# Performance work log

Hardware: AMD Instinct MI355X
Metric: run time of the kernel (lower is better)

The kernel has to match this reference:

```python
import jax, jax.numpy as jnp
import numpy as np

B, H, W, C = 32, 56, 56, 512
HEADS, WS, SS = 16, 7, 3
N = WS * WS            # window area = 49
HD = C // HEADS        # head dim = 32
HID = 4 * C            # mlp hidden = 2048
nWh, nWw = H // WS, W // WS
nW = nWh * nWw


def _rel_pos_index():
    # static (N, N) int index into relative_position_bias_table
    coords = np.stack(np.meshgrid(np.arange(WS), np.arange(WS), indexing='ij'))  # (2, WS, WS)
    cf = coords.reshape(2, -1)                       # (2, N)
    rel = (cf[:, :, None] - cf[:, None, :]).transpose(1, 2, 0).copy()  # (N, N, 2)
    rel[:, :, 0] += WS - 1
    rel[:, :, 1] += WS - 1
    rel[:, :, 0] *= 2 * WS - 1
    return rel.sum(-1)  # (N, N)


def _attn_mask():
    # static shifted-window attention mask, (nW, N, N) with 0 / -100
    img = np.zeros((H, W))
    cnt = 0
    for h0, h1 in ((0, H - WS), (H - WS, H - SS), (H - SS, H)):
        for w0, w1 in ((0, W - WS), (W - WS, W - SS), (W - SS, W)):
            img[h0:h1, w0:w1] = cnt
            cnt += 1
    mw = img.reshape(nWh, WS, nWw, WS).transpose(0, 2, 1, 3).reshape(-1, N)  # (nW, N)
    diff = mw[:, None, :] - mw[:, :, None]
    return np.where(diff != 0, -100.0, 0.0).astype(np.float32)

_REL_IDX = _rel_pos_index()
_MASK = _attn_mask()


def _ln(x, g, b, eps=1e-5):
    mu = x.mean(-1, keepdims=True)
    var = ((x - mu) ** 2).mean(-1, keepdims=True)
    return (x - mu) * jax.lax.rsqrt(var + eps) * g + b


def setup_inputs() -> dict:
    key = jax.random.key(0)
    ks = jax.random.split(key, 8)
    s = lambda k, shape: jax.random.normal(k, shape, jnp.float32) * 0.02
    return {
        'x': jax.random.normal(ks[0], (B, H, W, C), jnp.float32),
        'norm1_g': jnp.ones((C,), jnp.float32), 'norm1_b': jnp.zeros((C,), jnp.float32),
        'qkv_w': s(ks[1], (3 * C, C)), 'qkv_b': jnp.zeros((3 * C,), jnp.float32),
        'rel_pos_table': s(ks[2], ((2 * WS - 1) ** 2, HEADS)),
        'proj_w': s(ks[3], (C, C)), 'proj_b': jnp.zeros((C,), jnp.float32),
        'norm2_g': jnp.ones((C,), jnp.float32), 'norm2_b': jnp.zeros((C,), jnp.float32),
        'fc1_w': s(ks[4], (HID, C)), 'fc1_b': jnp.zeros((HID,), jnp.float32),
        'fc2_w': s(ks[5], (C, HID)), 'fc2_b': jnp.zeros((C,), jnp.float32),
    }


def reference(x, norm1_g, norm1_b, qkv_w, qkv_b, rel_pos_table, proj_w, proj_b,
              norm2_g, norm2_b, fc1_w, fc1_b, fc2_w, fc2_b):
    shortcut = x
    y = _ln(x, norm1_g, norm1_b)
    # cyclic shift
    y = jnp.roll(y, (-SS, -SS), axis=(1, 2))
    # window partition -> (B*nW, N, C)
    yw = y.reshape(B, nWh, WS, nWw, WS, C).transpose(0, 1, 3, 2, 4, 5).reshape(B * nW, N, C)
    # qkv projection
    qkv = yw @ qkv_w.T + qkv_b
    qkv = qkv.reshape(B * nW, N, 3, HEADS, HD).transpose(2, 0, 3, 1, 4)
    q, k, v = qkv[0], qkv[1], qkv[2]              # each (B*nW, HEADS, N, HD)
    scale = HD ** -0.5
    attn = jnp.einsum('bhqd,bhkd->bhqk', q * scale, k)  # (B*nW, HEADS, N, N)
    # relative position bias gather
    bias = rel_pos_table[jnp.asarray(_REL_IDX.reshape(-1))].reshape(N, N, HEADS)
    attn = attn + bias.transpose(2, 0, 1)[None]
    # shifted-window mask
    attn = attn.reshape(B, nW, HEADS, N, N) + jnp.asarray(_MASK)[None, :, None]
    attn = jax.nn.softmax(attn.reshape(B * nW, HEADS, N, N), axis=-1)
    o = jnp.einsum('bhqk,bhkd->bhqd', attn, v)
    o = o.transpose(0, 2, 1, 3).reshape(B * nW, N, C)
    o = o @ proj_w.T + proj_b
    # window reverse + reverse shift
    o = o.reshape(B, nWh, nWw, WS, WS, C).transpose(0, 1, 3, 2, 4, 5).reshape(B, H, W, C)
    o = jnp.roll(o, (SS, SS), axis=(1, 2))
    x = shortcut + o
    # MLP
    h = _ln(x, norm2_g, norm2_b)
    h = jax.nn.gelu(h @ fc1_w.T + fc1_b, approximate=False)
    h = h @ fc2_w.T + fc2_b
    return x + h
```

## Files before the change

### kernel.cpp

```cpp
#include <hip/hip_runtime.h>

#define Bb   32
#define Hh   56
#define Ww_  56
#define Cc   512
#define HEADS 16
#define WS   7
#define SS   3
#define Nn   49
#define HD   32
#define HID  2048
#define NWIN 2048
#define NTOK 100352
#define NTOKP 100416

typedef __attribute__((ext_vector_type(4))) float f32x4;
typedef __attribute__((ext_vector_type(8))) short bf16x8;

#define AS1 __attribute__((address_space(1)))
#define AS3 __attribute__((address_space(3)))

__device__ __forceinline__ ushort f2bf(float x) {
  union { float f; unsigned u; } un; un.f = x;
  unsigned u = un.u;
  return (ushort)((u + 0x7fffu + ((u >> 16) & 1u)) >> 16);
}

__device__ __forceinline__ void cvt_frag_seg(const float* __restrict__ s, ushort* __restrict__ d,
                                             int N, int K, int tid0, int stride) {
  int nch = (N * K) >> 3;
  int kc = K >> 3;
  int kkt = K >> 5;
  for (int c = tid0; c < nch; c += stride) {
    int row = c / kc, col8 = c - row * kc;
    int n0 = row >> 4, l15 = row & 15;
    int kk = col8 >> 2, lhi = col8 & 3;
    int lane = (lhi << 4) | l15;
    const float* sp = s + (size_t)c * 8;
    ushort* dp = d + (((size_t)(n0 * kkt + kk) * 64 + lane) * 8);
    #pragma unroll
    for (int e = 0; e < 8; ++e) dp[e] = f2bf(sp[e]);
  }
}

__global__ void cvtwf_kern(const float* __restrict__ s0, ushort* __restrict__ d0,
                           const float* __restrict__ s1, ushort* __restrict__ d1,
                           const float* __restrict__ s2, ushort* __restrict__ d2,
                           const float* __restrict__ s3, ushort* __restrict__ d3) {
  int tid0 = blockIdx.x * 256 + threadIdx.x;
  int stride = gridDim.x * 256;
  cvt_frag_seg(s0, d0, 1536, 512, tid0, stride);
  cvt_frag_seg(s1, d1, 512, 512, tid0, stride);
  cvt_frag_seg(s2, d2, 2048, 512, tid0, stride);
  cvt_frag_seg(s3, d3, 512, 2048, tid0, stride);
}

__global__ void prep_bias_kern(const float* __restrict__ table, float* __restrict__ be2) {
  int idx = blockIdx.x * 256 + threadIdx.x;
  int h = idx >> 12, q = (idx >> 6) & 63, t = idx & 63;
  int l15 = t >> 2, n = t & 3;
  int key = n * 16 + l15;
  float v = 0.f;
  if (q < Nn && key < Nn) {
    int qi = q / 7, qj = q - qi * 7;
    int ki = key / 7, kj = key - ki * 7;
    v = table[((qi - ki + 6) * 13 + (qj - kj + 6)) * HEADS + h];
  }
  be2[idx] = v;
}

template<int MODE>
__global__ __launch_bounds__(256) void ln_kern(const float* __restrict__ x,
    const float* __restrict__ g, const float* __restrict__ bsh,
    ushort* __restrict__ out)
{
  int row  = blockIdx.x * 4 + (threadIdx.x >> 6);
  int lane = threadIdx.x & 63;
  const float* src;
  if (MODE == 0) {
    unsigned w = (unsigned)row / 49u, n = (unsigned)row - w * 49u;
    unsigned bb = w >> 6, wi = w & 63;
    unsigned wh = wi >> 3, ww = wi & 7;
    unsigned i = n / 7u, j = n - i * 7u;
    unsigned sr = wh * 7 + i + SS; if (sr >= Hh) sr -= Hh;
    unsigned sc = ww * 7 + j + SS; if (sc >= Ww_) sc -= Ww_;
    src = x + ((size_t)(bb * Hh + sr) * Ww_ + sc) * Cc;
  } else {
    src = x + (size_t)row * Cc;
  }
  int c = lane * 8;
  f32x4 v0 = *(const f32x4*)(src + c);
  f32x4 v1 = *(const f32x4*)(src + c + 4);
  float s = 0.f, s2 = 0.f;
  #pragma unroll
  for (int e = 0; e < 4; ++e) { s += v0[e]; s2 += v0[e]*v0[e]; s += v1[e]; s2 += v1[e]*v1[e]; }
  #pragma unroll
  for (int off = 32; off; off >>= 1) { s += __shfl_xor(s, off); s2 += __shfl_xor(s2, off); }
  float mu = s * (1.f / 512.f);
  float rstd = rsqrtf(s2 * (1.f / 512.f) - mu * mu + 1e-5f);
  bf16x8 r;
  #pragma unroll
  for (int e = 0; e < 8; ++e) {
    float xv = (e < 4) ? v0[e] : v1[e - 4];
    r[e] = (short)f2bf((xv - mu) * rstd * g[c + e] + bsh[c + e]);
  }
  *(bf16x8*)(out + (size_t)row * Cc + c) = r;
}

template<int EPI>
__global__ __launch_bounds__(256, 2) void gemm_kern(
    const ushort* __restrict__ A, const ushort* __restrict__ Bf,
    const float* __restrict__ bias, int M, int N, int K,
    void* __restrict__ outp, const float* __restrict__ resid,
    ushort* __restrict__ qb, ushort* __restrict__ kb, ushort* __restrict__ vb)
{
  __shared__ ushort As[2][128 * 64];
  const int tid = threadIdx.x;
  const int wave = tid >> 6, lane = tid & 63;
  const int l15 = lane & 15, lhi = lane >> 4;
  const int sw7 = l15 & 7;

  int gx = gridDim.x;
  int nwg = gx * gridDim.y;
  int orig = blockIdx.y * gx + blockIdx.x;
  int cpx = nwg >> 3;
  int wg = (orig & 7) * cpx + (orig >> 3);
  int bx = wg % gx, by = wg / gx;
  const int brow = by * 128, bcol = bx * 128;

  const int wr = (wave >> 1) * 64, wc = (wave & 1) * 64;

  const int srow = lane >> 3;
  const int schk = ((lane & 7) ^ srow) * 8;
  const ushort* aG = A + (size_t)(brow + srow) * K + schk;

  const int kkt = K >> 5;
  const int nb0 = (bcol + wc) >> 4;
  const ushort* bW = Bf + (size_t)nb0 * kkt * 512 + (size_t)lane * 8;

  auto stageA = [&](int kt, int sl) {
    #pragma unroll
    for (int s = 0; s < 4; ++s) {
      int rg = (s * 4 + wave) * 8;
      __builtin_amdgcn_global_load_lds(
        (const AS1 void*)(aG + (size_t)rg * K + kt * 64),
        (AS3 void*)&As[sl][rg * 64], 16, 0, 0);
    }
  };

  f32x4 acc[4][4];
  #pragma unroll
  for (int m = 0; m < 4; ++m)
    #pragma unroll
    for (int n = 0; n < 4; ++n)
      acc[m][n] = (f32x4){0.f, 0.f, 0.f, 0.f};

  const int nt = K >> 6;

  stageA(0, 0);
  __syncthreads();

  for (int t = 0; t < nt; ++t) {
    const int sl = t & 1;
    bf16x8 bfr[2][4];
    #pragma unroll
    for (int kk = 0; kk < 2; ++kk)
      #pragma unroll
      for (int n = 0; n < 4; ++n)
        bfr[kk][n] = *(const bf16x8*)(bW + ((size_t)n * kkt + t * 2 + kk) * 512);
    if (t + 1 < nt) stageA(t + 1, sl ^ 1);
    const ushort* Ap = As[sl];
    #pragma unroll
    for (int kk = 0; kk < 2; ++kk) {
      bf16x8 af[4];
      #pragma unroll
      for (int m = 0; m < 4; ++m)
        af[m] = *(const bf16x8*)&Ap[(wr + m * 16 + l15) * 64 + (((kk * 4 + lhi) ^ sw7)) * 8];
      #pragma unroll
      for (int m = 0; m < 4; ++m)
        #pragma unroll
        for (int n = 0; n < 4; ++n)
          acc[m][n] = __builtin_amdgcn_mfma_f32_16x16x32_bf16(af[m], bfr[kk][n], acc[m][n], 0, 0, 0);
    }
    __syncthreads();
  }

  float bv[4];
  #pragma unroll
  for (int n = 0; n < 4; ++n) bv[n] = bias[bcol + wc + n * 16 + l15];
  #pragma unroll
  for (int m = 0; m < 4; ++m) {
    int rbase = brow + wr + m * 16 + lhi * 4;
    #pragma unroll
    for (int n = 0; n < 4; ++n) {
      int cc = bcol + wc + n * 16 + l15;
      #pragma unroll
      for (int j = 0; j < 4; ++j) {
        unsigned r = (unsigned)(rbase + j);
        float v = acc[m][n][j] + bv[n];
        if (EPI == 0) {
          int part = cc >> 9, head = (cc >> 5) & 15, d = cc & 31;
          ushort bvs = f2bf(v);
          if (part == 0)      qb[((size_t)head * NTOKP + r) * 32 + d] = bvs;
          else if (part == 1) kb[((size_t)head * NTOKP + r) * 32 + d] = bvs;
          else {
            unsigned w = r / 49u, nn = r - w * 49u;
            vb[(((size_t)(w * HEADS + head)) * 32 + d) * 64 + nn] = bvs;
          }
        } else if (EPI == 1) {
          float u2 = v * (1.5957691216f + 0.0713548162f * v * v);
          float gl = __fdividef(v, 1.0f + __expf(-u2));
          ((ushort*)outp)[(size_t)r * N + cc] = f2bf(gl);
        } else if (EPI == 2) {
          unsigned w = r / 49u, nn = r - w * 49u;
          unsigned bb = w >> 6, wi = w & 63;
          unsigned wh = wi >> 3, ww = wi & 7;
          unsigned ii = nn / 7u, jj = nn - ii * 7u;
          unsigned dr = wh * 7 + ii + SS; if (dr >= Hh) dr -= Hh;
          unsigned dc = ww * 7 + jj + SS; if (dc >= Ww_) dc -= Ww_;
          size_t p = ((size_t)bb * Hh + dr) * Ww_ + dc;
          ((float*)outp)[p * Cc + cc] = resid[p * Cc + cc] + v;
        } else {
          float* o = (float*)outp;
          size_t idx = (size_t)r * Cc + cc;
          o[idx] = o[idx] + v;
        }
      }
    }
  }
}

__global__ __launch_bounds__(256) void attn_kern(
    const ushort* __restrict__ qb, const ushort* __restrict__ kb,
    const ushort* __restrict__ vb, const float* __restrict__ be2,
    ushort* __restrict__ o_win)
{
  __shared__ ushort P[4][4096];
  const int wv = threadIdx.x >> 6, lane = threadIdx.x & 63;
  const int l15 = lane & 15, lhi = lane >> 4;
  const int w = blockIdx.x;
  const int head = blockIdx.y * 4 + wv;
  const int wi = w & 63, whh = wi >> 3, www = wi & 7;
  ushort* Pl = P[wv];

  int krg[4];
  #pragma unroll
  for (int n = 0; n < 4; ++n) {
    int key = n * 16 + l15;
    int rg = -1;
    if (key < Nn) {
      int ki = key / 7, kj = key - ki * 7;
      int rr = whh * 7 + ki, cc = www * 7 + kj;
      rg = (rr < 49 ? 0 : (rr < 53 ? 1 : 2)) * 3 + (cc < 49 ? 0 : (cc < 53 ? 1 : 2));
    }
    krg[n] = rg;
  }
  int qrg[4][4];
  #pragma unroll
  for (int m = 0; m < 4; ++m)
    #pragma unroll
    for (int j = 0; j < 4; ++j) {
      int q = m * 16 + lhi * 4 + j;
      int rg = -2;
      if (q < Nn) {
        int qi = q / 7, qj = q - qi * 7;
        int rr = whh * 7 + qi, cc = www * 7 + qj;
        rg = (rr < 49 ? 0 : (rr < 53 ? 1 : 2)) * 3 + (cc < 49 ? 0 : (cc < 53 ? 1 : 2));
      }
      qrg[m][j] = rg;
    }

  const ushort* qp = qb + ((size_t)head * NTOKP + (size_t)w * 49) * 32;
  const ushort* kp = kb + ((size_t)head * NTOKP + (size_t)w * 49) * 32;
  const ushort* vp = vb + (size_t)(w * HEADS + head) * 2048;
  const float*  bep = be2 + head * 4096;

  bf16x8 qf[4], kf[4];
  #pragma unroll
  for (int m = 0; m < 4; ++m) {
    qf[m] = *(const bf16x8*)(qp + (m * 16 + l15) * 32 + lhi * 8);
    kf[m] = *(const bf16x8*)(kp + (m * 16 + l15) * 32 + lhi * 8);
  }
  f32x4 sa[4][4];
  #pragma unroll
  for (int m = 0; m < 4; ++m)
    #pragma unroll
    for (int n = 0; n < 4; ++n)
      sa[m][n] = __builtin_amdgcn_mfma_f32_16x16x32_bf16(qf[m], kf[n],
                   (f32x4){0.f, 0.f, 0.f, 0.f}, 0, 0, 0);

  #pragma unroll
  for (int m = 0; m < 4; ++m)
    #pragma unroll
    for (int j = 0; j < 4; ++j) {
      int q = m * 16 + lhi * 4 + j;
      int qr = qrg[m][j];
      f32x4 bev = *(const f32x4*)(bep + q * 64 + l15 * 4);
      float vv[4];
      float mx = -1e30f;
      #pragma unroll
      for (int n = 0; n < 4; ++n) {
        float v;
        if (qr >= 0 && krg[n] >= 0) {
          v = sa[m][n][j] * 0.17677669529663687f + bev[n];
          if (qr != krg[n]) v -= 100.0f;
        } else v = -1e30f;
        vv[n] = v;
        mx = fmaxf(mx, v);
      }
      #pragma unroll
      for (int off = 8; off; off >>= 1) mx = fmaxf(mx, __shfl_xor(mx, off));
      float sum = 0.f;
      #pragma unroll
      for (int n = 0; n < 4; ++n) { float p = __expf(vv[n] - mx); vv[n] = p; sum += p; }
      #pragma unroll
      for (int off = 8; off; off >>= 1) sum += __shfl_xor(sum, off);
      float is = 1.0f / sum;
      #pragma unroll
      for (int n = 0; n < 4; ++n) {
        int bo = (q * 128 + (n * 16 + l15) * 2) ^ ((q & 7) << 4);
        *(ushort*)((char*)Pl + bo) = f2bf(vv[n] * is);
      }
    }

  bf16x8 vf[2][2];
  #pragma unroll
  for (int nt = 0; nt < 2; ++nt)
    #pragma unroll
    for (int kt = 0; kt < 2; ++kt)
      vf[nt][kt] = *(const bf16x8*)(vp + (nt * 16 + l15) * 64 + kt * 32 + lhi * 8);
  f32x4 oa[4][2];
  #pragma unroll
  for (int m = 0; m < 4; ++m)
    #pragma unroll
    for (int nt = 0; nt < 2; ++nt)
      oa[m][nt] = (f32x4){0.f, 0.f, 0.f, 0.f};
  #pragma unroll
  for (int m = 0; m < 4; ++m) {
    int row = m * 16 + l15;
    #pragma unroll
    for (int kt = 0; kt < 2; ++kt) {
      int bo = (row * 128 + kt * 64 + lhi * 16) ^ ((row & 7) << 4);
      bf16x8 pa = *(const bf16x8*)((char*)Pl + bo);
      #pragma unroll
      for (int nt = 0; nt < 2; ++nt)
        oa[m][nt] = __builtin_amdgcn_mfma_f32_16x16x32_bf16(pa, vf[nt][kt], oa[m][nt], 0, 0, 0);
    }
  }
  #pragma unroll
  for (int m = 0; m < 4; ++m) {
    int q0 = m * 16 + lhi * 4;
    #pragma unroll
    for (int nt = 0; nt < 2; ++nt) {
      int d = nt * 16 + l15;
      #pragma unroll
      for (int j = 0; j < 4; ++j) {
        int q = q0 + j;
        if (q < Nn)
          o_win[((size_t)w * Nn + q) * Cc + head * HD + d] = f2bf(oa[m][nt][j]);
      }
    }
  }
}

extern "C" void kernel_launch(void* const* d_in, const int* in_sizes, int n_in,
                              void* d_out, int out_size, void* d_ws, size_t ws_size,
                              hipStream_t stream) {
  const float* x      = (const float*)d_in[0];
  const float* n1g    = (const float*)d_in[1];
  const float* n1b    = (const float*)d_in[2];
  const float* qkv_w  = (const float*)d_in[3];
  const float* qkv_b  = (const float*)d_in[4];
  const float* relt   = (const float*)d_in[5];
  const float* proj_w = (const float*)d_in[6];
  const float* proj_b = (const float*)d_in[7];
  const float* n2g    = (const float*)d_in[8];
  const float* n2b    = (const float*)d_in[9];
  const float* fc1_w  = (const float*)d_in[10];
  const float* fc1_b  = (const float*)d_in[11];
  const float* fc2_w  = (const float*)d_in[12];
  const float* fc2_b  = (const float*)d_in[13];

  char* ws = (char*)d_ws;
  ushort* wq = (ushort*)ws; ws += (size_t)1536 * 512 * 2;
  ushort* wp = (ushort*)ws; ws += (size_t)512 * 512 * 2;
  ushort* w1 = (ushort*)ws; ws += (size_t)2048 * 512 * 2;
  ushort* w2 = (ushort*)ws; ws += (size_t)512 * 2048 * 2;
  float*  be = (float*)ws;  ws += (size_t)16 * 64 * 64 * 4;
  ushort* buf1 = (ushort*)ws; ws += (size_t)NTOK * 2048 * 2;
  ushort* qbuf = (ushort*)ws; ws += (size_t)16 * NTOKP * 32 * 2;
  ushort* kbuf = (ushort*)ws; ws += (size_t)16 * NTOKP * 32 * 2;
  ushort* vbuf = (ushort*)ws; ws += (size_t)NWIN * 16 * 32 * 64 * 2;
  ushort* yw = buf1;
  ushort* o_win = buf1;
  ushort* h1 = buf1;
  ushort* l2buf = qbuf;
  float* xout = (float*)d_out;

  cvtwf_kern<<<2048, 256, 0, stream>>>(qkv_w, wq, proj_w, wp, fc1_w, w1, fc2_w, w2);
  prep_bias_kern<<<65536 / 256, 256, 0, stream>>>(relt, be);

  ln_kern<0><<<NTOK / 4, 256, 0, stream>>>(x, n1g, n1b, yw);
  gemm_kern<0><<<dim3(12, 784), 256, 0, stream>>>(yw, wq, qkv_b, NTOK, 1536, 512,
                                                  nullptr, nullptr, qbuf, kbuf, vbuf);
  attn_kern<<<dim3(NWIN, 4), 256, 0, stream>>>(qbuf, kbuf, vbuf, be, o_win);
  gemm_kern<2><<<dim3(4, 784), 256, 0, stream>>>(o_win, wp, proj_b, NTOK, 512, 512,
                                                 xout, x, nullptr, nullptr, nullptr);
  ln_kern<1><<<NTOK / 4, 256, 0, stream>>>(xout, n2g, n2b, l2buf);
  gemm_kern<1><<<dim3(16, 784), 256, 0, stream>>>(l2buf, w1, fc1_b, NTOK, 2048, 512,
                                                  h1, nullptr, nullptr, nullptr, nullptr);
  gemm_kern<3><<<dim3(4, 784), 256, 0, stream>>>(h1, w2, fc2_b, NTOK, 512, 2048,
                                                 xout, xout, nullptr, nullptr, nullptr);
}
```

Measured before the change: 1.300 ms.

## Store GEMM A operands in MFMA-fragment tiled layout and load directly

Changes the layout of every GEMM A operand (LN output, attention output, GELU hidden) to a 16-row by 8-column blocked format matching the MFMA fragment, so each lane can load its A fragment straight from global memory. This removes the LDS staging, double buffer, swizzle and per-iteration __syncthreads in the GEMM. The trade-off is that A tiles are no longer shared through LDS, so the two waves covering the same rows each fetch them from global/L2. Producer epilogues now write scattered 16-byte or 2-byte chunks in the new layout.

```diff
diff --git a/kernel.cpp b/kernel.cpp
--- a/kernel.cpp
+++ b/kernel.cpp
@@ -104,21 +104,19 @@
     float xv = (e < 4) ? v0[e] : v1[e - 4];
     r[e] = (short)f2bf((xv - mu) * rstd * g[c + e] + bsh[c + e]);
   }
-  *(bf16x8*)(out + (size_t)row * Cc + c) = r;
+  *(bf16x8*)(out + ((size_t)(row >> 4) * 64 + lane) * 128 + (row & 15) * 8) = r;
 }
 
 template<int EPI>
 __global__ __launch_bounds__(256, 2) void gemm_kern(
-    const ushort* __restrict__ A, const ushort* __restrict__ Bf,
+    const ushort* __restrict__ A2, const ushort* __restrict__ Bf,
     const float* __restrict__ bias, int M, int N, int K,
     void* __restrict__ outp, const float* __restrict__ resid,
     ushort* __restrict__ qb, ushort* __restrict__ kb, ushort* __restrict__ vb)
 {
-  __shared__ ushort As[2][128 * 64];
   const int tid = threadIdx.x;
   const int wave = tid >> 6, lane = tid & 63;
   const int l15 = lane & 15, lhi = lane >> 4;
-  const int sw7 = l15 & 7;
 
   int gx = gridDim.x;
   int nwg = gx * gridDim.y;
@@ -130,23 +128,15 @@
 
   const int wr = (wave >> 1) * 64, wc = (wave & 1) * 64;
 
-  const int srow = lane >> 3;
-  const int schk = ((lane & 7) ^ srow) * 8;
-  const ushort* aG = A + (size_t)(brow + srow) * K + schk;
-
+  const int kc8 = K >> 3;
   const int kkt = K >> 5;
   const int nb0 = (bcol + wc) >> 4;
   const ushort* bW = Bf + (size_t)nb0 * kkt * 512 + (size_t)lane * 8;
 
-  auto stageA = [&](int kt, int sl) {
-    #pragma unroll
-    for (int s = 0; s < 4; ++s) {
-      int rg = (s * 4 + wave) * 8;
-      __builtin_amdgcn_global_load_lds(
-        (const AS1 void*)(aG + (size_t)rg * K + kt * 64),
-        (AS3 void*)&As[sl][rg * 64], 16, 0, 0);
-    }
-  };
+  const ushort* aB[4];
+  #pragma unroll
+  for (int m = 0; m < 4; ++m)
+    aB[m] = A2 + ((size_t)((unsigned)(brow + wr + m * 16) >> 4) * kc8 + lhi) * 128 + l15 * 8;
 
   f32x4 acc[4][4];
   #pragma unroll
@@ -157,32 +147,25 @@
 
   const int nt = K >> 6;
 
-  stageA(0, 0);
-  __syncthreads();
-
   for (int t = 0; t < nt; ++t) {
-    const int sl = t & 1;
-    bf16x8 bfr[2][4];
+    bf16x8 bfr[2][4], af[2][4];
     #pragma unroll
     for (int kk = 0; kk < 2; ++kk)
       #pragma unroll
       for (int n = 0; n < 4; ++n)
         bfr[kk][n] = *(const bf16x8*)(bW + ((size_t)n * kkt + t * 2 + kk) * 512);
-    if (t + 1 < nt) stageA(t + 1, sl ^ 1);
-    const ushort* Ap = As[sl];
-    #pragma unroll
-    for (int kk = 0; kk < 2; ++kk) {
-      bf16x8 af[4];
+    #pragma unroll
+    for (int kk = 0; kk < 2; ++kk)
       #pragma unroll
       for (int m = 0; m < 4; ++m)
-        af[m] = *(const bf16x8*)&Ap[(wr + m * 16 + l15) * 64 + (((kk * 4 + lhi) ^ sw7)) * 8];
+        af[kk][m] = *(const bf16x8*)(aB[m] + (size_t)(t * 8 + kk * 4) * 128);
+    #pragma unroll
+    for (int kk = 0; kk < 2; ++kk)
       #pragma unroll
       for (int m = 0; m < 4; ++m)
         #pragma unroll
         for (int n = 0; n < 4; ++n)
-          acc[m][n] = __builtin_amdgcn_mfma_f32_16x16x32_bf16(af[m], bfr[kk][n], acc[m][n], 0, 0, 0);
-    }
-    __syncthreads();
+          acc[m][n] = __builtin_amdgcn_mfma_f32_16x16x32_bf16(af[kk][m], bfr[kk][n], acc[m][n], 0, 0, 0);
   }
 
   float bv[4];
@@ -191,6 +174,7 @@
   #pragma unroll
   for (int m = 0; m < 4; ++m) {
     int rbase = brow + wr + m * 16 + lhi * 4;
+    size_t hb = (size_t)((unsigned)(brow + wr + m * 16) >> 4) * (N >> 3);
     #pragma unroll
     for (int n = 0; n < 4; ++n) {
       int cc = bcol + wc + n * 16 + l15;
@@ -210,7 +194,7 @@
         } else if (EPI == 1) {
           float u2 = v * (1.5957691216f + 0.0713548162f * v * v);
           float gl = __fdividef(v, 1.0f + __expf(-u2));
-          ((ushort*)outp)[(size_t)r * N + cc] = f2bf(gl);
+          ((ushort*)outp)[(hb + (cc >> 3)) * 128 + (lhi * 4 + j) * 8 + (cc & 7)] = f2bf(gl);
         } else if (EPI == 2) {
           unsigned w = r / 49u, nn = r - w * 49u;
           unsigned bb = w >> 6, wi = w & 63;
@@ -352,12 +336,14 @@
     int q0 = m * 16 + lhi * 4;
     #pragma unroll
     for (int nt = 0; nt < 2; ++nt) {
-      int d = nt * 16 + l15;
       #pragma unroll
       for (int j = 0; j < 4; ++j) {
         int q = q0 + j;
-        if (q < Nn)
-          o_win[((size_t)w * Nn + q) * Cc + head * HD + d] = f2bf(oa[m][nt][j]);
+        if (q < Nn) {
+          unsigned tok = (unsigned)(w * 49 + q);
+          o_win[((size_t)(tok >> 4) * 64 + head * 4 + nt * 2 + (l15 >> 3)) * 128
+                + (tok & 15) * 8 + (l15 & 7)] = f2bf(oa[m][nt][j]);
+        }
       }
     }
   }
```

Measured after the change: 2.015 ms. +55.0%, slower.
